# Kernel tuning notes

Hardware: AMD Instinct MI355X
Metric: run time of the kernel (lower is better)

The kernel has to match this reference:

```python
import jax, jax.numpy as jnp
import numpy as np

T, B, D_IN, D_HID = 512, 256, 256, 256  # n_qubits == hidden_dim


def setup_inputs() -> dict:
    key = jax.random.key(0)
    ks = jax.random.split(key, 9)
    d_comb = D_IN + D_HID
    inp = {"inputs": jax.random.normal(ks[0], (T, B, D_IN), dtype=jnp.float32)}
    names = ["f", "i", "g", "o"]
    for j, n in enumerate(names):
        inp[f"W{n}"] = jax.random.normal(ks[1 + 2 * j], (D_HID, d_comb), dtype=jnp.float32) * 0.02
        inp[f"b{n}"] = jax.random.normal(ks[2 + 2 * j], (D_HID,), dtype=jnp.float32) * 0.02
        inp[f"t{n}"] = jnp.float32(1.0)
    return inp


def _qgate(comb, W, b, temp):
    # Linear -> RY angles; RY product state + CNOT chain gives
    # <Z_k> = prod_{i<=k} cos(theta_i)  (closed form of the circuit)
    theta = comb @ W.T + b                      # [B, n_qubits]
    return jnp.cumprod(jnp.cos(theta), axis=-1) / temp


def reference(inputs, Wf, bf, tf, Wi, bi, ti, Wg, bg, tg, Wo, bo, to):
    B_ = inputs.shape[1]
    h0 = jnp.zeros((B_, D_HID), dtype=inputs.dtype)
    c0 = jnp.zeros((B_, D_HID), dtype=inputs.dtype)

    def step(carry, x):
        hx, cx = carry
        comb = jnp.concatenate([x, hx], axis=1)          # [B, D_IN+D_HID]
        f = jax.nn.sigmoid(_qgate(comb, Wf, bf, tf))
        i = jax.nn.sigmoid(_qgate(comb, Wi, bi, ti))
        g = jnp.tanh(_qgate(comb, Wg, bg, tg))
        o = jax.nn.sigmoid(_qgate(comb, Wo, bo, to))
        cx = f * cx + i * g
        hx = o * jnp.tanh(cx)   # dropout in eval mode = identity
        return (hx, cx), hx

    (hx, cx), outs = jax.lax.scan(step, (h0, c0), inputs)
    return outs, hx, cx
```

## Files before the change

kernel.cpp:

```cpp
#include <hip/hip_runtime.h>

#define T_STEPS 512
#define BATCH   256
#define DIN     256
#define DHID    256
#define NWG     256
#define NTHREADS 512

typedef short bf16_t;
typedef __attribute__((ext_vector_type(4))) short short4v;
typedef __attribute__((ext_vector_type(8))) short short8;
typedef __attribute__((ext_vector_type(4))) float f32x4;
typedef __attribute__((ext_vector_type(4))) int int32x4;
typedef unsigned int uint;
typedef unsigned short ushort;

#define WS_WXP  0u
#define WS_WHQ  (512u << 10)
#define WS_SW   (768u << 10)
#define WS_RQ   (772u << 10)
#define WS_BIAS (776u << 10)
#define WS_TMP  (780u << 10)
#define WS_HGQ  (784u << 10)
#define WS_CG   (848u << 10)
#define WS_THX  (2u << 20)

#define TXSTEPU 131072

__device__ inline short f2bf(float f) {
  union { float f; uint u; } v; v.f = f;
  uint r = (v.u + 0x7FFFu + ((v.u >> 16) & 1u)) >> 16;
  return (short)r;
}
__device__ inline float bf2fu(ushort s) {
  union { float f; uint u; } v; v.u = ((uint)s) << 16;
  return v.f;
}
__device__ inline float u2f(uint u) {
  union { float f; uint u; } v; v.u = u; return v.f;
}
__device__ inline float frcp(float x) { return __builtin_amdgcn_rcpf(x); }
__device__ inline float fast_sigmoid(float x) { return frcp(1.f + __expf(-x)); }
__device__ inline float fast_tanh(float x) {
  float ax = fabsf(x);
  float e = __expf(2.f * ax);
  float r = 1.f - 2.f * frcp(e + 1.f);
  return copysignf(r, x);
}

__device__ inline void mfma_i8_a(int32x4& acc, int32x4 a, int32x4 b) {
  asm("v_mfma_i32_16x16x64_i8 %0, %1, %2, %0"
      : "+v"(acc) : "v"(a), "a"(b));
}

__global__ __launch_bounds__(256) void k_scales(
    const float* __restrict__ Wf, const float* __restrict__ Wi,
    const float* __restrict__ Wg, const float* __restrict__ Wo,
    float* __restrict__ sw, float* __restrict__ rq)
{
  int n = blockIdx.x * 256 + threadIdx.x;
  int gate = n >> 8, nrow = n & 255;
  const float* W = gate == 0 ? Wf : gate == 1 ? Wi : gate == 2 ? Wg : Wo;
  const float4* row = (const float4*)(W + (size_t)nrow * 512 + 256);
  float amax = 0.f;
#pragma unroll 4
  for (int k = 0; k < 64; ++k) {
    float4 v = row[k];
    amax = fmaxf(amax, fmaxf(fmaxf(fabsf(v.x), fabsf(v.y)),
                             fmaxf(fabsf(v.z), fabsf(v.w))));
  }
  sw[n] = amax / (127.f * 127.f);
  rq[n] = amax > 0.f ? 127.f / amax : 0.f;
}

__global__ __launch_bounds__(256) void k_packx(
    const float* __restrict__ Wf, const float* __restrict__ Wi,
    const float* __restrict__ Wg, const float* __restrict__ Wo,
    const float* __restrict__ bf_, const float* __restrict__ bi_,
    const float* __restrict__ bg_, const float* __restrict__ bo_,
    const float* __restrict__ tf_, const float* __restrict__ ti_,
    const float* __restrict__ tg_, const float* __restrict__ to_,
    bf16_t* __restrict__ Wxp, float* __restrict__ bias,
    float* __restrict__ temps)
{
  int tid = blockIdx.x * 256 + threadIdx.x;
  int nt = tid >> 9;
  int kt = (tid >> 6) & 7;
  int lane = tid & 63;
  int n = nt * 16 + (lane & 15);
  int gate = n >> 8, nrow = n & 255;
  int k = kt * 32 + (lane >> 4) * 8;
  const float* W = gate == 0 ? Wf : gate == 1 ? Wi : gate == 2 ? Wg : Wo;
  const float* src = W + (size_t)nrow * 512 + k;
  short8 d;
#pragma unroll
  for (int j = 0; j < 8; ++j) d[j] = f2bf(src[j]);
  *(short8*)(Wxp + (size_t)tid * 8) = d;

  if (tid < 1024) {
    int g2 = tid >> 8;
    const float* bs = g2 == 0 ? bf_ : g2 == 1 ? bi_ : g2 == 2 ? bg_ : bo_;
    bias[tid] = bs[tid & 255];
  }
  if (tid < 4) {
    const float* ts = tid == 0 ? tf_ : tid == 1 ? ti_ : tid == 2 ? tg_ : to_;
    temps[tid] = ts[0];
  }
}

__global__ __launch_bounds__(256) void k_packh(
    const float* __restrict__ Wf, const float* __restrict__ Wi,
    const float* __restrict__ Wg, const float* __restrict__ Wo,
    const float* __restrict__ rq, signed char* __restrict__ Whq)
{
  int tid = blockIdx.x * 256 + threadIdx.x;
  int nt = tid >> 8;
  int kt = (tid >> 6) & 3;
  int lane = tid & 63;
  int fc = lane & 15;
  int gate = nt >> 4, hh = (nt >> 3) & 1, j = nt & 7;
  int n = gate * 256 + hh * 128 + ((j >> 1) << 5) + fc * 2 + (j & 1);
  int nrow = n & 255;
  int k0 = 256 + kt * 64 + (lane >> 4) * 16;
  const float* W = gate == 0 ? Wf : gate == 1 ? Wi : gate == 2 ? Wg : Wo;
  const float* src = W + (size_t)nrow * 512 + k0;
  float r = rq[n];
  union { signed char b[16]; int32x4 v; } pk;
#pragma unroll
  for (int jj = 0; jj < 16; ++jj) {
    int qi = __float2int_rn(src[jj] * r);
    qi = qi > 127 ? 127 : (qi < -127 ? -127 : qi);
    pk.b[jj] = (signed char)qi;
  }
  *(int32x4*)(Whq + (size_t)tid * 16) = pk.v;
}

__global__ __launch_bounds__(256, 1) void gemm_thx(
    const float* __restrict__ x,
    const bf16_t* __restrict__ Wxp,
    const float* __restrict__ bias,
    ushort* __restrict__ thxH)
{
  __shared__ bf16_t Ax[64 * 256];
  const int tid = threadIdx.x;
  const int wave = tid >> 6, lane = tid & 63;
  const int lg = lane >> 4, c = lane & 15;
  const int mb = blockIdx.x * 64;

#pragma unroll
  for (int rep = 0; rep < 16; ++rep) {
    int idx = tid + rep * 256;
    int row = idx >> 6, c4f = (idx & 63) * 4;
    float4 v = *(const float4*)(x + (size_t)(mb + row) * 256 + c4f);
    short4v d;
    d[0] = f2bf(v.x); d[1] = f2bf(v.y); d[2] = f2bf(v.z); d[3] = f2bf(v.w);
    *(short4v*)((char*)Ax + row * 512 + ((c4f * 2) ^ ((row & 7) << 4))) = d;
  }
  __syncthreads();

  short8 af[4][8];
#pragma unroll
  for (int mf = 0; mf < 4; ++mf)
#pragma unroll
    for (int kt = 0; kt < 8; ++kt) {
      int row = mf * 16 + (lane & 15);
      int kb = kt * 64 + (lane >> 4) * 16;
      af[mf][kt] = *(const short8*)((char*)Ax + row * 512 + (kb ^ ((row & 7) << 4)));
    }

#pragma unroll 1
  for (int i = 0; i < 16; ++i) {
    short8 wfr[8];
#pragma unroll
    for (int kt = 0; kt < 8; ++kt)
      wfr[kt] = *(const short8*)(Wxp + ((((size_t)(wave * 16 + i)) * 8 + kt) * 64 + lane) * 8);
    float bv = bias[wave * 256 + i * 16 + c];
    f32x4 ac[4];
#pragma unroll
    for (int mf = 0; mf < 4; ++mf) ac[mf] = (f32x4){0.f, 0.f, 0.f, 0.f};
#pragma unroll
    for (int kt = 0; kt < 8; ++kt)
#pragma unroll
      for (int mf = 0; mf < 4; ++mf)
        ac[mf] = __builtin_amdgcn_mfma_f32_16x16x32_bf16(af[mf][kt], wfr[kt], ac[mf], 0, 0, 0);
    const int kkg = i * 16 + c;
#pragma unroll
    for (int mf = 0; mf < 4; ++mf)
#pragma unroll
      for (int r = 0; r < 4; ++r) {
        int mrow = mb + mf * 16 + lg * 4 + r;
        int trel = mrow >> 8, rw = mrow & 255;
        thxH[(((size_t)trel * 256 + rw) * 4 + wave) * 256 + kkg] =
            (ushort)f2bf(ac[mf][r] + bv);
      }
  }
}

__global__ __launch_bounds__(NTHREADS, 2) void qlstm_rec(
    const uint* __restrict__ thxU,
    const int32x4* __restrict__ Whq,
    const float* __restrict__ sw,
    const float* __restrict__ temps,
    signed char* __restrict__ hGq, float* __restrict__ cG,
    float* __restrict__ out,
    int t0, int nsteps)
{
  __shared__ signed char A[16 * 256];
  __shared__ ushort ACT[4 * 264];
  __shared__ float halfTot[4];

  const int tid = threadIdx.x;
  const int wv = tid >> 6, lane = tid & 63;
  const int g = wv >> 1, hh = wv & 1;
  const int lg = lane >> 4, c = lane & 15;
  const int row = blockIdx.x;

  int32x4 w0[8], w3[8], wa1[8], wa2[8];
#pragma unroll
  for (int j = 0; j < 8; ++j) {
    const size_t nb = (size_t)(g * 16 + hh * 8 + j) * 4;
    w0[j]  = Whq[(nb + 0) * 64 + lane];
    wa1[j] = Whq[(nb + 1) * 64 + lane];
    wa2[j] = Whq[(nb + 2) * 64 + lane];
    w3[j]  = Whq[(nb + 3) * 64 + lane];
  }
  float s8j[8];
#pragma unroll
  for (int q = 0; q < 4; ++q) {
    float2 sv = *(const float2*)&sw[g * 256 + hh * 128 + q * 32 + c * 2];
    s8j[2 * q] = sv.x; s8j[2 * q + 1] = sv.y;
  }

  const float invt = frcp(temps[g]);
  const bool isg = (g == 2);

  const int e = tid >> 8, ukk = tid & 255;
  float creg = 0.f;
  {
    signed char hv = 0;
    if (t0 != 0) {
      hv = hGq[(size_t)row * 256 + ukk];
      creg = cG[(size_t)row * 256 + ukk];
    }
    const int r0 = e * 4, r1 = e * 4 + 8;
    A[r0 * 256 + (ukk ^ ((r0 & 7) << 4))] = hv;
    A[r1 * 256 + (ukk ^ ((r1 & 7) << 4))] = hv;
  }
  __syncthreads();

  const size_t txbase = (((size_t)row * 4 + g) * 128) + hh * 64 + lane;
  uint tx = thxU[txbase];

#pragma unroll 1
  for (int ts = 0; ts < nsteps; ++ts) {
    const int t = t0 + ts;
    const bool last = (ts == nsteps - 1);

    const int tsn = (ts + 1 < nsteps) ? ts + 1 : ts;
    const uint txn = thxU[(size_t)tsn * TXSTEPU + txbase];

    int32x4 af[4];
#pragma unroll
    for (int kt = 0; kt < 4; ++kt)
      af[kt] = *(const int32x4*)&A[c * 256 + ((kt * 64 + lg * 16) ^ ((c & 7) << 4))];

    int32x4 acc[8];
#pragma unroll
    for (int j = 0; j < 8; ++j) {
      acc[j] = (int32x4){0, 0, 0, 0};
      acc[j] = __builtin_amdgcn_mfma_i32_16x16x64_i8(af[0], w0[j], acc[j], 0, 0, 0);
    }
#pragma unroll
    for (int j = 0; j < 8; ++j) mfma_i8_a(acc[j], af[1], wa1[j]);
#pragma unroll
    for (int j = 0; j < 8; ++j) mfma_i8_a(acc[j], af[2], wa2[j]);
#pragma unroll
    for (int j = 0; j < 8; ++j)
      acc[j] = __builtin_amdgcn_mfma_i32_16x16x64_i8(af[3], w3[j], acc[j], 0, 0, 0);

    float d0 = (float)acc[0][0] * s8j[0], d1 = (float)acc[1][0] * s8j[1];
    float d2 = (float)acc[2][0] * s8j[2], d3 = (float)acc[3][0] * s8j[3];
    float d4 = (float)acc[4][0] * s8j[4], d5 = (float)acc[5][0] * s8j[5];
    float d6 = (float)acc[6][0] * s8j[6], d7 = (float)acc[7][0] * s8j[7];
    float v0 = lg == 0 ? d0 : lg == 1 ? d2 : lg == 2 ? d4 : d6;
    float v1 = lg == 0 ? d1 : lg == 1 ? d3 : lg == 2 ? d5 : d7;

    float c0 = __cosf(u2f(tx << 16) + v0);
    float c1 = __cosf(u2f(tx & 0xffff0000u) + v1);
    float pair = c0 * c1;

    float incl = pair;
#pragma unroll
    for (int d = 1; d < 64; d <<= 1) {
      float o = __shfl_up(incl, d);
      if (lane >= d) incl *= o;
    }
    float prefix = __shfl_up(incl, 1);
    if (lane == 0) prefix = 1.f;
    if (hh == 0 && lane == 63) halfTot[g] = incl;
    __syncthreads();
    if (hh) prefix *= halfTot[g];

    float r0v = prefix * c0;
    float a0 = isg ? fast_tanh(r0v * invt) : fast_sigmoid(r0v * invt);
    float r1v = r0v * c1;
    float a1 = isg ? fast_tanh(r1v * invt) : fast_sigmoid(r1v * invt);
    uint pk = (uint)(ushort)f2bf(a0) | ((uint)(ushort)f2bf(a1) << 16);
    *(uint*)&ACT[g * 264 + hh * 128 + lane * 2] = pk;
    __syncthreads();

    {
      float fv = bf2fu(ACT[0 * 264 + ukk]);
      float iv = bf2fu(ACT[1 * 264 + ukk]);
      float gv = bf2fu(ACT[2 * 264 + ukk]);
      float ov = bf2fu(ACT[3 * 264 + ukk]);
      float cn = fv * creg + iv * gv;
      creg = cn;
      float h = ov * fast_tanh(cn);
      int hq = __float2int_rn(h * 127.f);
      const int r0 = e * 4, r1 = e * 4 + 8;
      A[r0 * 256 + (ukk ^ ((r0 & 7) << 4))] = (signed char)hq;
      A[r1 * 256 + (ukk ^ ((r1 & 7) << 4))] = (signed char)hq;
      if (e == 0) {
        out[((size_t)t * BATCH + row) * DHID + ukk] = h;
        if (t == T_STEPS - 1) {
          out[((size_t)T_STEPS * BATCH + row) * DHID + ukk] = h;
          out[((size_t)T_STEPS * BATCH + BATCH + row) * DHID + ukk] = cn;
        }
        if (last) {
          hGq[(size_t)row * 256 + ukk] = (signed char)hq;
          cG[(size_t)row * 256 + ukk] = cn;
        }
      }
    }
    __syncthreads();

    tx = txn;
  }
}

extern "C" void kernel_launch(void* const* d_in, const int* in_sizes, int n_in,
                              void* d_out, int out_size, void* d_ws, size_t ws_size,
                              hipStream_t stream) {
  (void)in_sizes; (void)n_in; (void)out_size;
  const float* x   = (const float*)d_in[0];
  const float* Wf  = (const float*)d_in[1];
  const float* bf_ = (const float*)d_in[2];
  const float* tf_ = (const float*)d_in[3];
  const float* Wi  = (const float*)d_in[4];
  const float* bi_ = (const float*)d_in[5];
  const float* ti_ = (const float*)d_in[6];
  const float* Wg  = (const float*)d_in[7];
  const float* bg_ = (const float*)d_in[8];
  const float* tg_ = (const float*)d_in[9];
  const float* Wo  = (const float*)d_in[10];
  const float* bo_ = (const float*)d_in[11];
  const float* to_ = (const float*)d_in[12];

  char* ws = (char*)d_ws;
  bf16_t*      Wxp   = (bf16_t*)(ws + WS_WXP);
  signed char* Whq   = (signed char*)(ws + WS_WHQ);
  float*       sw    = (float*)(ws + WS_SW);
  float*       rq    = (float*)(ws + WS_RQ);
  float*       bias  = (float*)(ws + WS_BIAS);
  float*       temps = (float*)(ws + WS_TMP);
  signed char* hGq   = (signed char*)(ws + WS_HGQ);
  float*       cG    = (float*)(ws + WS_CG);
  ushort*      thxH  = (ushort*)(ws + WS_THX);

  size_t avail = ws_size > (size_t)(2u << 20) ? ws_size - (size_t)(2u << 20) : 0;
  int CH = 4;
  const int cands[6] = {128, 64, 32, 16, 8, 4};
  for (int ci = 0; ci < 6; ++ci)
    if ((size_t)cands[ci] * 512 * 1024 <= avail) { CH = cands[ci]; break; }

  hipLaunchKernelGGL(k_scales, dim3(4), dim3(256), 0, stream,
                     Wf, Wi, Wg, Wo, sw, rq);
  hipLaunchKernelGGL(k_packx, dim3(128), dim3(256), 0, stream,
                     Wf, Wi, Wg, Wo, bf_, bi_, bg_, bo_, tf_, ti_, tg_, to_,
                     Wxp, bias, temps);
  hipLaunchKernelGGL(k_packh, dim3(64), dim3(256), 0, stream,
                     Wf, Wi, Wg, Wo, rq, Whq);

  for (int c0 = 0; c0 < T_STEPS; c0 += CH) {
    hipLaunchKernelGGL(gemm_thx, dim3(CH * 4), dim3(256), 0, stream,
                       x + (size_t)c0 * BATCH * DIN, Wxp, bias, thxH);
    hipLaunchKernelGGL(qlstm_rec, dim3(NWG), dim3(NTHREADS), 0, stream,
                       (const uint*)thxH, (const int32x4*)Whq, sw, temps,
                       hGq, cG, (float*)d_out, c0, CH);
  }
}
```

Measured before the change: 991.4 us.

## Split hidden state into two int8 halves and merge activation into single barrier

Quantizes h to roughly 15 bits as high and low int8 parts and runs twice the int8 MFMAs per step, raising recurrent precision. The input projection is now stored as fp16 instead of bf16. The prefix product now uses DPP row operations instead of shfl_up, and the gate activations move into the cell-update threads, which removes one __syncthreads per step. The h output store is deferred by one step. The cost is doubled MFMA work on the serial critical path in exchange for one fewer barrier and cheaper scans.

```diff
diff --git a/kernel.cpp b/kernel.cpp
--- a/kernel.cpp
+++ b/kernel.cpp
@@ -22,22 +22,22 @@
 #define WS_BIAS (776u << 10)
 #define WS_TMP  (780u << 10)
 #define WS_HGQ  (784u << 10)
-#define WS_CG   (848u << 10)
+#define WS_CG   (912u << 10)
 #define WS_THX  (2u << 20)
 
 #define TXSTEPU 131072
+#define HSCALE  32512.f
 
 __device__ inline short f2bf(float f) {
   union { float f; uint u; } v; v.f = f;
   uint r = (v.u + 0x7FFFu + ((v.u >> 16) & 1u)) >> 16;
   return (short)r;
 }
-__device__ inline float bf2fu(ushort s) {
-  union { float f; uint u; } v; v.u = ((uint)s) << 16;
-  return v.f;
-}
-__device__ inline float u2f(uint u) {
-  union { float f; uint u; } v; v.u = u; return v.f;
+__device__ inline ushort f2h(float f) {
+  union { _Float16 h; ushort u; } v; v.h = (_Float16)f; return v.u;
+}
+__device__ inline float h2f(ushort u) {
+  union { _Float16 h; ushort u; } v; v.u = u; return (float)v.h;
 }
 __device__ inline float frcp(float x) { return __builtin_amdgcn_rcpf(x); }
 __device__ inline float fast_sigmoid(float x) { return frcp(1.f + __expf(-x)); }
@@ -52,6 +52,10 @@
   asm("v_mfma_i32_16x16x64_i8 %0, %1, %2, %0"
       : "+v"(acc) : "v"(a), "a"(b));
 }
+
+#define DPPM(x, ctrl, rmask)                                                  \
+  __int_as_float(__builtin_amdgcn_update_dpp(                                 \
+      0x3f800000, __float_as_int(x), (ctrl), (rmask), 0xf, false))
 
 __global__ __launch_bounds__(256) void k_scales(
     const float* __restrict__ Wf, const float* __restrict__ Wi,
@@ -69,7 +73,7 @@
     amax = fmaxf(amax, fmaxf(fmaxf(fabsf(v.x), fabsf(v.y)),
                              fmaxf(fabsf(v.z), fabsf(v.w))));
   }
-  sw[n] = amax / (127.f * 127.f);
+  sw[n] = amax / (127.f * HSCALE);
   rq[n] = amax > 0.f ? 127.f / amax : 0.f;
 }
 
@@ -191,7 +195,7 @@
         int mrow = mb + mf * 16 + lg * 4 + r;
         int trel = mrow >> 8, rw = mrow & 255;
         thxH[(((size_t)trel * 256 + rw) * 4 + wave) * 256 + kkg] =
-            (ushort)f2bf(ac[mf][r] + bv);
+            f2h(ac[mf][r] + bv);
       }
   }
 }
@@ -205,15 +209,16 @@
     float* __restrict__ out,
     int t0, int nsteps)
 {
-  __shared__ signed char A[16 * 256];
-  __shared__ ushort ACT[4 * 264];
-  __shared__ float halfTot[4];
+  __shared__ signed char Hq[512];
+  __shared__ float RAW[4 * 264];
+  __shared__ __align__(16) float halfTot[4];
 
   const int tid = threadIdx.x;
   const int wv = tid >> 6, lane = tid & 63;
   const int g = wv >> 1, hh = wv & 1;
-  const int lg = lane >> 4, c = lane & 15;
+  const int lg = lane >> 4;
   const int row = blockIdx.x;
+  const int ukk = tid & 255, e = tid >> 8;
 
   int32x4 w0[8], w3[8], wa1[8], wa2[8];
 #pragma unroll
@@ -224,118 +229,139 @@
     wa2[j] = Whq[(nb + 2) * 64 + lane];
     w3[j]  = Whq[(nb + 3) * 64 + lane];
   }
-  float s8j[8];
-#pragma unroll
-  for (int q = 0; q < 4; ++q) {
-    float2 sv = *(const float2*)&sw[g * 256 + hh * 128 + q * 32 + c * 2];
-    s8j[2 * q] = sv.x; s8j[2 * q + 1] = sv.y;
-  }
-
-  const float invt = frcp(temps[g]);
-  const bool isg = (g == 2);
-
-  const int e = tid >> 8, ukk = tid & 255;
+  const float2 sc = *(const float2*)&sw[g * 256 + hh * 128 + lane * 2];
+  const float it0 = frcp(temps[0]), it1 = frcp(temps[1]);
+  const float it2 = frcp(temps[2]), it3 = frcp(temps[3]);
+
   float creg = 0.f;
   {
-    signed char hv = 0;
+    signed char hvh = 0, hvl = 0;
     if (t0 != 0) {
-      hv = hGq[(size_t)row * 256 + ukk];
+      hvh = hGq[(size_t)row * 256 + ukk];
+      hvl = hGq[65536 + (size_t)row * 256 + ukk];
       creg = cG[(size_t)row * 256 + ukk];
     }
-    const int r0 = e * 4, r1 = e * 4 + 8;
-    A[r0 * 256 + (ukk ^ ((r0 & 7) << 4))] = hv;
-    A[r1 * 256 + (ukk ^ ((r1 & 7) << 4))] = hv;
+    if (e == 0) { Hq[ukk] = hvh; Hq[256 + ukk] = hvl; }
   }
   __syncthreads();
 
-  const size_t txbase = (((size_t)row * 4 + g) * 128) + hh * 64 + lane;
+  const size_t txbase = ((size_t)row * 4 + g) * 128 + hh * 64 + lane;
   uint tx = thxU[txbase];
+  float hprev = 0.f, cprev = 0.f;
 
 #pragma unroll 1
   for (int ts = 0; ts < nsteps; ++ts) {
     const int t = t0 + ts;
-    const bool last = (ts == nsteps - 1);
+
+    if (ts > 0 && e == 0)
+      out[((size_t)(t - 1) * BATCH + row) * DHID + ukk] = hprev;
 
     const int tsn = (ts + 1 < nsteps) ? ts + 1 : ts;
     const uint txn = thxU[(size_t)tsn * TXSTEPU + txbase];
 
-    int32x4 af[4];
-#pragma unroll
-    for (int kt = 0; kt < 4; ++kt)
-      af[kt] = *(const int32x4*)&A[c * 256 + ((kt * 64 + lg * 16) ^ ((c & 7) << 4))];
-
-    int32x4 acc[8];
-#pragma unroll
-    for (int j = 0; j < 8; ++j) {
-      acc[j] = (int32x4){0, 0, 0, 0};
-      acc[j] = __builtin_amdgcn_mfma_i32_16x16x64_i8(af[0], w0[j], acc[j], 0, 0, 0);
-    }
-#pragma unroll
-    for (int j = 0; j < 8; ++j) mfma_i8_a(acc[j], af[1], wa1[j]);
-#pragma unroll
-    for (int j = 0; j < 8; ++j) mfma_i8_a(acc[j], af[2], wa2[j]);
+    int32x4 afh0 = *(const int32x4*)&Hq[lg * 16];
+    int32x4 afh1 = *(const int32x4*)&Hq[lg * 16 + 64];
+    int32x4 afh2 = *(const int32x4*)&Hq[lg * 16 + 128];
+    int32x4 afh3 = *(const int32x4*)&Hq[lg * 16 + 192];
+    int32x4 afl0 = *(const int32x4*)&Hq[256 + lg * 16];
+    int32x4 afl1 = *(const int32x4*)&Hq[256 + lg * 16 + 64];
+    int32x4 afl2 = *(const int32x4*)&Hq[256 + lg * 16 + 128];
+    int32x4 afl3 = *(const int32x4*)&Hq[256 + lg * 16 + 192];
+
+    const int32x4 zq = {0, 0, 0, 0};
+    int32x4 acch[8], accl[8];
 #pragma unroll
     for (int j = 0; j < 8; ++j)
-      acc[j] = __builtin_amdgcn_mfma_i32_16x16x64_i8(af[3], w3[j], acc[j], 0, 0, 0);
-
-    float d0 = (float)acc[0][0] * s8j[0], d1 = (float)acc[1][0] * s8j[1];
-    float d2 = (float)acc[2][0] * s8j[2], d3 = (float)acc[3][0] * s8j[3];
-    float d4 = (float)acc[4][0] * s8j[4], d5 = (float)acc[5][0] * s8j[5];
-    float d6 = (float)acc[6][0] * s8j[6], d7 = (float)acc[7][0] * s8j[7];
-    float v0 = lg == 0 ? d0 : lg == 1 ? d2 : lg == 2 ? d4 : d6;
-    float v1 = lg == 0 ? d1 : lg == 1 ? d3 : lg == 2 ? d5 : d7;
-
-    float c0 = __cosf(u2f(tx << 16) + v0);
-    float c1 = __cosf(u2f(tx & 0xffff0000u) + v1);
+      acch[j] = __builtin_amdgcn_mfma_i32_16x16x64_i8(afh0, w0[j], zq, 0, 0, 0);
+#pragma unroll
+    for (int j = 0; j < 8; ++j)
+      accl[j] = __builtin_amdgcn_mfma_i32_16x16x64_i8(afl0, w0[j], zq, 0, 0, 0);
+#pragma unroll
+    for (int j = 0; j < 8; ++j) mfma_i8_a(acch[j], afh1, wa1[j]);
+#pragma unroll
+    for (int j = 0; j < 8; ++j) mfma_i8_a(accl[j], afl1, wa1[j]);
+#pragma unroll
+    for (int j = 0; j < 8; ++j) mfma_i8_a(acch[j], afh2, wa2[j]);
+#pragma unroll
+    for (int j = 0; j < 8; ++j) mfma_i8_a(accl[j], afl2, wa2[j]);
+#pragma unroll
+    for (int j = 0; j < 8; ++j)
+      acch[j] = __builtin_amdgcn_mfma_i32_16x16x64_i8(afh3, w3[j], acch[j], 0, 0, 0);
+#pragma unroll
+    for (int j = 0; j < 8; ++j)
+      accl[j] = __builtin_amdgcn_mfma_i32_16x16x64_i8(afl3, w3[j], accl[j], 0, 0, 0);
+
+    int ah0 = (lg < 2) ? (lg == 0 ? acch[0][0] : acch[2][0])
+                       : (lg == 2 ? acch[4][0] : acch[6][0]);
+    int ah1 = (lg < 2) ? (lg == 0 ? acch[1][0] : acch[3][0])
+                       : (lg == 2 ? acch[5][0] : acch[7][0]);
+    int al0 = (lg < 2) ? (lg == 0 ? accl[0][0] : accl[2][0])
+                       : (lg == 2 ? accl[4][0] : accl[6][0]);
+    int al1 = (lg < 2) ? (lg == 0 ? accl[1][0] : accl[3][0])
+                       : (lg == 2 ? accl[5][0] : accl[7][0]);
+    float th0 = (float)((ah0 << 8) + al0) * sc.x;
+    float th1 = (float)((ah1 << 8) + al1) * sc.y;
+    float c0 = __cosf(h2f((ushort)(tx & 0xffffu)) + th0);
+    float c1 = __cosf(h2f((ushort)(tx >> 16)) + th1);
     float pair = c0 * c1;
 
-    float incl = pair;
-#pragma unroll
-    for (int d = 1; d < 64; d <<= 1) {
-      float o = __shfl_up(incl, d);
-      if (lane >= d) incl *= o;
-    }
+    float s = pair;
+    s *= DPPM(s, 0x111, 0xf);
+    s *= DPPM(s, 0x112, 0xf);
+    s *= DPPM(s, 0x114, 0xf);
+    s *= DPPM(s, 0x118, 0xf);
+    s *= DPPM(s, 0x142, 0xa);
+    s *= DPPM(s, 0x143, 0xc);
+    const float incl = s;
     float prefix = __shfl_up(incl, 1);
     if (lane == 0) prefix = 1.f;
+
+    float2 rw; rw.x = prefix * c0; rw.y = incl;
+    *(float2*)&RAW[g * 264 + hh * 128 + lane * 2] = rw;
     if (hh == 0 && lane == 63) halfTot[g] = incl;
     __syncthreads();
-    if (hh) prefix *= halfTot[g];
-
-    float r0v = prefix * c0;
-    float a0 = isg ? fast_tanh(r0v * invt) : fast_sigmoid(r0v * invt);
-    float r1v = r0v * c1;
-    float a1 = isg ? fast_tanh(r1v * invt) : fast_sigmoid(r1v * invt);
-    uint pk = (uint)(ushort)f2bf(a0) | ((uint)(ushort)f2bf(a1) << 16);
-    *(uint*)&ACT[g * 264 + hh * 128 + lane * 2] = pk;
-    __syncthreads();
 
     {
-      float fv = bf2fu(ACT[0 * 264 + ukk]);
-      float iv = bf2fu(ACT[1 * 264 + ukk]);
-      float gv = bf2fu(ACT[2 * 264 + ukk]);
-      float ov = bf2fu(ACT[3 * 264 + ukk]);
+      float r_f = RAW[0 * 264 + ukk], r_i = RAW[1 * 264 + ukk];
+      float r_g = RAW[2 * 264 + ukk], r_o = RAW[3 * 264 + ukk];
+      if (ukk >= 128) {
+        float4 hT = *(const float4*)halfTot;
+        r_f *= hT.x; r_i *= hT.y; r_g *= hT.z; r_o *= hT.w;
+      }
+      float fv = fast_sigmoid(r_f * it0);
+      float iv = fast_sigmoid(r_i * it1);
+      float gv = fast_tanh  (r_g * it2);
+      float ov = fast_sigmoid(r_o * it3);
       float cn = fv * creg + iv * gv;
       creg = cn;
       float h = ov * fast_tanh(cn);
-      int hq = __float2int_rn(h * 127.f);
-      const int r0 = e * 4, r1 = e * 4 + 8;
-      A[r0 * 256 + (ukk ^ ((r0 & 7) << 4))] = (signed char)hq;
-      A[r1 * 256 + (ukk ^ ((r1 & 7) << 4))] = (signed char)hq;
       if (e == 0) {
-        out[((size_t)t * BATCH + row) * DHID + ukk] = h;
-        if (t == T_STEPS - 1) {
-          out[((size_t)T_STEPS * BATCH + row) * DHID + ukk] = h;
-          out[((size_t)T_STEPS * BATCH + BATCH + row) * DHID + ukk] = cn;
-        }
-        if (last) {
-          hGq[(size_t)row * 256 + ukk] = (signed char)hq;
-          cG[(size_t)row * 256 + ukk] = cn;
-        }
+        int q = __float2int_rn(h * HSCALE);
+        int lo = ((q + 128) & 255) - 128;
+        int hi = (q - lo) >> 8;
+        Hq[ukk] = (signed char)hi;
+        Hq[256 + ukk] = (signed char)lo;
+        hprev = h; cprev = cn;
       }
     }
     __syncthreads();
 
     tx = txn;
+  }
+
+  if (e == 0) {
+    const int tl = t0 + nsteps - 1;
+    out[((size_t)tl * BATCH + row) * DHID + ukk] = hprev;
+    if (tl == T_STEPS - 1) {
+      out[((size_t)T_STEPS * BATCH + row) * DHID + ukk] = hprev;
+      out[((size_t)T_STEPS * BATCH + BATCH + row) * DHID + ukk] = cprev;
+    }
+    int q = __float2int_rn(hprev * HSCALE);
+    int lo = ((q + 128) & 255) - 128;
+    int hi = (q - lo) >> 8;
+    hGq[(size_t)row * 256 + ukk] = (signed char)hi;
+    hGq[65536 + (size_t)row * 256 + ukk] = (signed char)lo;
+    cG[(size_t)row * 256 + ukk] = cprev;
   }
 }
 
```

Result: slower. 1.119 ms, median of 2 (+12.9%).
